# Performance work log

Hardware: AMD Instinct MI355X
Metric: run time of the kernel (lower is better)

Reference implementation:

```python
import jax, jax.numpy as jnp
import numpy as np

B, N, D_MODEL, HIDDEN = 4, 1024, 1024, 1024
N_HEAD, D_KEY, D_VALUE = 16, 64, 64


def setup_inputs() -> dict:
    key = jax.random.key(0)
    ks = jax.random.split(key, 12)
    s = 0.02
    return {
        "queries": jax.random.normal(ks[0], (B, N, D_MODEL), jnp.float32),
        "keys": jax.random.normal(ks[1], (B, N, HIDDEN), jnp.float32),
        "values": jax.random.normal(ks[2], (B, N, HIDDEN), jnp.float32),
        "attn_bias": jax.random.normal(ks[3], (B, N_HEAD, N, N), jnp.float32),
        "Wq": jax.random.normal(ks[4], (D_MODEL, D_KEY * N_HEAD), jnp.float32) * s,
        "bq": jnp.zeros((D_KEY * N_HEAD,), jnp.float32),
        "Wk": jax.random.normal(ks[5], (HIDDEN, D_KEY * N_HEAD), jnp.float32) * s,
        "bk": jnp.zeros((D_KEY * N_HEAD,), jnp.float32),
        "Wv": jax.random.normal(ks[6], (HIDDEN, D_VALUE * N_HEAD), jnp.float32) * s,
        "bv": jnp.zeros((D_VALUE * N_HEAD,), jnp.float32),
        "Wo": jax.random.normal(ks[7], (max(D_MODEL, HIDDEN), D_MODEL), jnp.float32) * s,
        "bo": jnp.zeros((D_MODEL,), jnp.float32),
    }


def reference(queries, keys, values, attn_bias, Wq, bq, Wk, bk, Wv, bv, Wo, bo):
    b, n, _ = queries.shape
    # QKV projections, split heads -> [b, h, n, d]
    q = (queries @ Wq + bq).reshape(b, n, N_HEAD, D_KEY).transpose(0, 2, 1, 3)
    k = (keys @ Wk + bk).reshape(b, keys.shape[1], N_HEAD, D_KEY).transpose(0, 2, 1, 3)
    v = (values @ Wv + bv).reshape(b, values.shape[1], N_HEAD, D_VALUE).transpose(0, 2, 1, 3)
    # scaled dot-product attention with additive bias (dropout_rate=0 -> identity)
    scaled_q = q * (D_KEY ** -0.5)
    product = jnp.einsum("bhqd,bhkd->bhqk", scaled_q, k) + attn_bias
    weights = jax.nn.softmax(product, axis=-1)
    ctx = jnp.einsum("bhqk,bhkd->bhqd", weights, v)
    # combine heads -> [b, n, h*d]
    out = ctx.transpose(0, 2, 1, 3).reshape(b, n, N_HEAD * D_VALUE)
    return out @ Wo + bo
```

## Files before the change

### kernel.cpp

```cpp
#include <hip/hip_runtime.h>
#include <cstdint>
#include <type_traits>


typedef unsigned short u16;
typedef __attribute__((ext_vector_type(8))) short v8bf;
typedef __attribute__((ext_vector_type(4))) float v4f;

#define DEV static __device__ __forceinline__

DEV u16 f2b(float f) {
    union { float f; uint32_t u; } v; v.f = f;
    uint32_t r = v.u + 0x7FFFu + ((v.u >> 16) & 1u);
    return (u16)(r >> 16);
}

DEV void gl_lds16(const void* g, void* l) {
    __builtin_amdgcn_global_load_lds((const __attribute__((address_space(1))) void*)g,
                                     (__attribute__((address_space(3))) void*)l, 16, 0, 0);
}

__global__ __launch_bounds__(256) void transpose_w4(const float* __restrict__ w0, const float* __restrict__ w1,
                                                    const float* __restrict__ w2, const float* __restrict__ w3,
                                                    u16* __restrict__ o0, u16* __restrict__ o1,
                                                    u16* __restrict__ o2, u16* __restrict__ o3) {
    __shared__ float tile[32][33];
    const float* in = blockIdx.z == 0 ? w0 : blockIdx.z == 1 ? w1 : blockIdx.z == 2 ? w2 : w3;
    u16* out        = blockIdx.z == 0 ? o0 : blockIdx.z == 1 ? o1 : blockIdx.z == 2 ? o2 : o3;
    const int tx = threadIdx.x, ty = threadIdx.y;
    const int n0 = blockIdx.x * 32, k0 = blockIdx.y * 32;
#pragma unroll
    for (int i = 0; i < 4; i++)
        tile[ty + i * 8][tx] = in[(size_t)(k0 + ty + i * 8) * 1024 + n0 + tx];
    __syncthreads();
#pragma unroll
    for (int i = 0; i < 4; i++)
        out[(size_t)(n0 + ty + i * 8) * 1024 + k0 + tx] = f2b(tile[tx][ty + i * 8]);
}

__global__ __launch_bounds__(256) void cast3(const float* __restrict__ a0, const float* __restrict__ a1,
                                             const float* __restrict__ a2,
                                             u16* __restrict__ o0, u16* __restrict__ o1, u16* __restrict__ o2) {
    const int z = blockIdx.y;
    const float* in = z == 0 ? a0 : z == 1 ? a1 : a2;
    u16* out        = z == 0 ? o0 : z == 1 ? o1 : o2;
    const size_t i = ((size_t)blockIdx.x * 256 + threadIdx.x) * 8;
    const float4 f0 = *reinterpret_cast<const float4*>(in + i);
    const float4 f1 = *reinterpret_cast<const float4*>(in + i + 4);
    union { u16 h[8]; uint4 v4; } pk;
    pk.h[0] = f2b(f0.x); pk.h[1] = f2b(f0.y); pk.h[2] = f2b(f0.z); pk.h[3] = f2b(f0.w);
    pk.h[4] = f2b(f1.x); pk.h[5] = f2b(f1.y); pk.h[6] = f2b(f1.z); pk.h[7] = f2b(f1.w);
    *reinterpret_cast<uint4*>(out + i) = pk.v4;
}

template <int BN, typename TO>
DEV void gemm_body(const u16* __restrict__ A, const u16* __restrict__ Bt,
                   const float* __restrict__ bias, TO* __restrict__ C,
                   u16* __restrict__ Ct, float cscale, bool storeT,
                   u16* aS, u16* bS) {
    constexpr int FJ = BN / 32;
    const int tid = threadIdx.x;
    const int wave = tid >> 6, lane = tid & 63, l16 = lane & 15, quad = lane >> 4;
    const int m0 = blockIdx.x * 128, n0 = blockIdx.y * BN;
    const int wr = wave >> 1, wc = wave & 1;
    const int r8 = lane >> 3, c8 = lane & 7;

    v4f acc[4][FJ];
#pragma unroll
    for (int i = 0; i < 4; i++)
#pragma unroll
        for (int j = 0; j < FJ; j++) acc[i][j] = (v4f){0.f, 0.f, 0.f, 0.f};

    for (int kk = 0; kk < 1024; kk += 64) {
        if (kk) __syncthreads();
#pragma unroll
        for (int cl = 0; cl < 4; cl++) {
            const int row = wave * 32 + cl * 8 + r8;
            gl_lds16(A + (size_t)(m0 + row) * 1024 + kk + ((c8 ^ (row & 7)) * 8),
                     aS + (wave * 32 + cl * 8) * 64);
        }
#pragma unroll
        for (int cl = 0; cl < BN / 32; cl++) {
            const int row = wave * (BN / 4) + cl * 8 + r8;
            gl_lds16(Bt + (size_t)(n0 + row) * 1024 + kk + ((c8 ^ (row & 7)) * 8),
                     bS + (wave * (BN / 4) + cl * 8) * 64);
        }
        __syncthreads();
#pragma unroll
        for (int kt = 0; kt < 2; kt++) {
            v8bf af[4], bf[FJ];
#pragma unroll
            for (int i = 0; i < 4; i++) {
                const int row = wr * 64 + i * 16 + l16;
                af[i] = *reinterpret_cast<const v8bf*>(aS + row * 64 + (((kt * 4 + quad) ^ (row & 7)) * 8));
            }
#pragma unroll
            for (int j = 0; j < FJ; j++) {
                const int row = wc * (BN / 2) + j * 16 + l16;
                bf[j] = *reinterpret_cast<const v8bf*>(bS + row * 64 + (((kt * 4 + quad) ^ (row & 7)) * 8));
            }
#pragma unroll
            for (int i = 0; i < 4; i++)
#pragma unroll
                for (int j = 0; j < FJ; j++)
                    acc[i][j] = __builtin_amdgcn_mfma_f32_16x16x32_bf16(af[i], bf[j], acc[i][j], 0, 0, 0);
        }
    }
    float bv[FJ];
#pragma unroll
    for (int j = 0; j < FJ; j++) bv[j] = bias[n0 + wc * (BN / 2) + j * 16 + l16];
    if (storeT) {
#pragma unroll
        for (int i = 0; i < 4; i++)
#pragma unroll
            for (int j = 0; j < FJ; j++) {
                const int col = n0 + wc * (BN / 2) + j * 16 + l16;
                const int row0 = m0 + wr * 64 + i * 16 + quad * 4;
                union { u16 h[4]; uint2 u; } pk;
#pragma unroll
                for (int r = 0; r < 4; r++) pk.h[r] = f2b((acc[i][j][r] + bv[j]) * cscale);
                *reinterpret_cast<uint2*>(&Ct[(size_t)col * 4096 + row0]) = pk.u;
            }
    } else {
#pragma unroll
        for (int i = 0; i < 4; i++)
#pragma unroll
            for (int j = 0; j < FJ; j++) {
                const int col = n0 + wc * (BN / 2) + j * 16 + l16;
#pragma unroll
                for (int r = 0; r < 4; r++) {
                    const int row = m0 + wr * 64 + i * 16 + quad * 4 + r;
                    const float val = (acc[i][j][r] + bv[j]) * cscale;
                    if constexpr (std::is_same_v<TO, u16>) C[(size_t)row * 1024 + col] = f2b(val);
                    else                                   C[(size_t)row * 1024 + col] = val;
                }
            }
    }
}

__global__ __launch_bounds__(256, 3) void gemm_qkv(
    const u16* __restrict__ Qc, const u16* __restrict__ Kc, const u16* __restrict__ Vc,
    const u16* __restrict__ WqT, const u16* __restrict__ WkT, const u16* __restrict__ WvT,
    const float* __restrict__ bq, const float* __restrict__ bk, const float* __restrict__ bv,
    u16* __restrict__ Qb, u16* __restrict__ Kb, u16* __restrict__ VT) {
    __shared__ __align__(16) u16 aS[128 * 64];
    __shared__ __align__(16) u16 bS[128 * 64];
    const int z = blockIdx.z;
    const u16* A    = z == 0 ? Qc : z == 1 ? Kc : Vc;
    const u16* Bt   = z == 0 ? WqT : z == 1 ? WkT : WvT;
    const float* bi = z == 0 ? bq : z == 1 ? bk : bv;
    u16* Cn         = z == 0 ? Qb : Kb;
    gemm_body<128, u16>(A, Bt, bi, Cn, VT, z == 0 ? 0.125f : 1.0f, z == 2, aS, bS);
}

__global__ __launch_bounds__(256, 3) void gemm_out(const u16* __restrict__ A, const u16* __restrict__ Bt,
                                                   const float* __restrict__ bias, float* __restrict__ C) {
    __shared__ __align__(16) u16 aS[128 * 64];
    __shared__ __align__(16) u16 bS[64 * 64];
    gemm_body<64, float>(A, Bt, bias, C, nullptr, 1.0f, false, aS, bS);
}

__global__ __launch_bounds__(256, 3) void attn2(const u16* __restrict__ Q,
                                                const u16* __restrict__ K,
                                                const u16* __restrict__ VT,
                                                const float* __restrict__ bias,
                                                u16* __restrict__ ctx) {
    __shared__ __align__(16) u16 kS[64 * 64];
    __shared__ __align__(16) u16 vS[64 * 64];
    __shared__ __align__(16) float biasS[64 * 64];
    __shared__ __align__(16) u16 pT[4][16 * 72];

    const int tid = threadIdx.x;
    const int wave = tid >> 6, lane = tid & 63, l16 = lane & 15, quad = lane >> 4;
    const int q0 = blockIdx.x * 64, bh = blockIdx.y, b = bh >> 4, h = bh & 15;
    const int r8 = lane >> 3, c8 = lane & 7;
    const int r16 = lane >> 4, c16 = lane & 15;

    v8bf qf[2];
    {
        const size_t qrow = ((size_t)(b * 1024 + q0 + wave * 16 + l16)) * 1024 + h * 64;
        qf[0] = *reinterpret_cast<const v8bf*>(Q + qrow + quad * 8);
        qf[1] = *reinterpret_cast<const v8bf*>(Q + qrow + 32 + quad * 8);
    }

    v4f ctxacc[4];
#pragma unroll
    for (int v = 0; v < 4; v++) ctxacc[v] = (v4f){0.f, 0.f, 0.f, 0.f};
    float rs = 0.f;

    const size_t kg = ((size_t)b * 1024) * 1024 + h * 64;
    const size_t vg = ((size_t)h * 64) * 4096 + b * 1024;
    const float* bp = bias + ((size_t)bh * 1024 + q0) * 1024;
    u16* pw = pT[wave];

    for (int c = 0; c < 16; c++) {
        const int nc = c * 64;
        if (c) __syncthreads();
#pragma unroll
        for (int cl = 0; cl < 2; cl++) {
            const int key = wave * 16 + cl * 8 + r8;
            gl_lds16(K + kg + (size_t)(nc + key) * 1024 + ((c8 ^ (key & 7)) * 8),
                     kS + (wave * 16 + cl * 8) * 64);
        }
#pragma unroll
        for (int cl = 0; cl < 2; cl++) {
            const int d = wave * 16 + cl * 8 + r8;
            gl_lds16(VT + vg + (size_t)d * 4096 + nc + ((c8 ^ (d & 7)) * 8),
                     vS + (wave * 16 + cl * 8) * 64);
        }
#pragma unroll
        for (int cl = 0; cl < 4; cl++) {
            const int row = wave * 16 + cl * 4 + r16;
            gl_lds16(bp + (size_t)row * 1024 + nc + ((c16 ^ (row & 15)) * 4),
                     biasS + (wave * 16 + cl * 4) * 64);
        }
        __syncthreads();

#pragma unroll
        for (int t = 0; t < 4; t++) {
            v4f s = (v4f){0.f, 0.f, 0.f, 0.f};
#pragma unroll
            for (int kt = 0; kt < 2; kt++) {
                const int krow = t * 16 + l16;
                const v8bf kf = *reinterpret_cast<const v8bf*>(
                    kS + krow * 64 + (((kt * 4 + quad) ^ (krow & 7)) * 8));
                s = __builtin_amdgcn_mfma_f32_16x16x32_bf16(kf, qf[kt], s, 0, 0, 0);
            }
            const float4 bi = *reinterpret_cast<const float4*>(
                biasS + (wave * 16 + l16) * 64 + (((t * 4 + quad) ^ l16) * 4));
            const float p0 = __expf(s[0] + bi.x);
            const float p1 = __expf(s[1] + bi.y);
            const float p2 = __expf(s[2] + bi.z);
            const float p3 = __expf(s[3] + bi.w);
            rs += (p0 + p1) + (p2 + p3);
            union { u16 h[4]; uint2 u; } pk;
            pk.h[0] = f2b(p0); pk.h[1] = f2b(p1); pk.h[2] = f2b(p2); pk.h[3] = f2b(p3);
            *reinterpret_cast<uint2*>(pw + l16 * 72 + t * 16 + quad * 4) = pk.u;
        }
#pragma unroll
        for (int kt = 0; kt < 2; kt++) {
            const v8bf pf = *reinterpret_cast<const v8bf*>(pw + l16 * 72 + kt * 32 + quad * 8);
#pragma unroll
            for (int v = 0; v < 4; v++) {
                const int drow = v * 16 + l16;
                const v8bf vf = *reinterpret_cast<const v8bf*>(
                    vS + drow * 64 + (((kt * 4 + quad) ^ (drow & 7)) * 8));
                ctxacc[v] = __builtin_amdgcn_mfma_f32_16x16x32_bf16(pf, vf, ctxacc[v], 0, 0, 0);
            }
        }
    }

    rs += __shfl_xor(rs, 16);
    rs += __shfl_xor(rs, 32);
    float dninv[4];
#pragma unroll
    for (int r = 0; r < 4; r++) dninv[r] = 1.f / __shfl(rs, quad * 4 + r, 16);
#pragma unroll
    for (int v = 0; v < 4; v++)
#pragma unroll
        for (int r = 0; r < 4; r++) {
            const int row = q0 + wave * 16 + quad * 4 + r;
            ctx[((size_t)(b * 1024 + row)) * 1024 + h * 64 + v * 16 + l16] =
                f2b(ctxacc[v][r] * dninv[r]);
        }
}

extern "C" void kernel_launch(void* const* d_in, const int* in_sizes, int n_in,
                              void* d_out, int out_size, void* d_ws, size_t ws_size,
                              hipStream_t stream) {
    const float* queries = (const float*)d_in[0];
    const float* keys    = (const float*)d_in[1];
    const float* values  = (const float*)d_in[2];
    const float* abias   = (const float*)d_in[3];
    const float* Wq = (const float*)d_in[4];
    const float* bq = (const float*)d_in[5];
    const float* Wk = (const float*)d_in[6];
    const float* bk = (const float*)d_in[7];
    const float* Wv = (const float*)d_in[8];
    const float* bv = (const float*)d_in[9];
    const float* Wo = (const float*)d_in[10];
    const float* bo = (const float*)d_in[11];
    float* out = (float*)d_out;

    char* ws = (char*)d_ws;
    u16* Qb   = (u16*)(ws);
    u16* Kb   = (u16*)(ws + (size_t)(8u << 20));
    u16* VTb  = (u16*)(ws + (size_t)(16u << 20));
    u16* ctxb = (u16*)(ws + (size_t)(24u << 20));
    u16* Qc   = (u16*)(ws + (size_t)(32u << 20));
    u16* Kc   = (u16*)(ws + (size_t)(40u << 20));
    u16* Vc   = (u16*)(ws + (size_t)(48u << 20));
    u16* WqT  = (u16*)(ws + (size_t)(56u << 20));
    u16* WkT  = (u16*)(ws + (size_t)(58u << 20));
    u16* WvT  = (u16*)(ws + (size_t)(60u << 20));
    u16* WoT  = (u16*)(ws + (size_t)(62u << 20));

    transpose_w4<<<dim3(32, 32, 4), dim3(32, 8), 0, stream>>>(Wq, Wk, Wv, Wo, WqT, WkT, WvT, WoT);
    cast3<<<dim3(2048, 3), 256, 0, stream>>>(queries, keys, values, Qc, Kc, Vc);
    gemm_qkv<<<dim3(32, 8, 3), 256, 0, stream>>>(Qc, Kc, Vc, WqT, WkT, WvT, bq, bk, bv, Qb, Kb, VTb);
    attn2<<<dim3(16, 64), 256, 0, stream>>>(Qb, Kb, VTb, abias, ctxb);
    gemm_out<<<dim3(32, 16), 256, 0, stream>>>(ctxb, WoT, bo, out);
}
```

Baseline: 491.0 us.

## Double-buffer K/V/bias LDS tiles in attention and add MFMA priority hints

The attention kernel now keeps two LDS buffers for the K, V^T and bias tiles. It issues the async global-to-LDS loads for the next key chunk before computing on the current one, so each chunk needs one barrier instead of two and load latency overlaps with MFMA and exp work. s_setprio is raised around the MFMA sequences, and the grid is reordered so the head/batch index varies fastest. The larger LDS footprint lowers the occupancy bound from 3 to 2 blocks per CU, which costs some latency hiding.

```diff
diff --git a/kernel.cpp b/kernel.cpp
--- a/kernel.cpp
+++ b/kernel.cpp
@@ -160,19 +160,20 @@
     gemm_body<64, float>(A, Bt, bias, C, nullptr, 1.0f, false, aS, bS);
 }
 
-__global__ __launch_bounds__(256, 3) void attn2(const u16* __restrict__ Q,
+__global__ __launch_bounds__(256, 2) void attn2(const u16* __restrict__ Q,
                                                 const u16* __restrict__ K,
                                                 const u16* __restrict__ VT,
                                                 const float* __restrict__ bias,
                                                 u16* __restrict__ ctx) {
-    __shared__ __align__(16) u16 kS[64 * 64];
-    __shared__ __align__(16) u16 vS[64 * 64];
-    __shared__ __align__(16) float biasS[64 * 64];
+    __shared__ __align__(16) u16 kS[2][64 * 64];
+    __shared__ __align__(16) u16 vS[2][64 * 64];
+    __shared__ __align__(16) float biasS[2][64 * 64];
     __shared__ __align__(16) u16 pT[4][16 * 72];
 
     const int tid = threadIdx.x;
     const int wave = tid >> 6, lane = tid & 63, l16 = lane & 15, quad = lane >> 4;
-    const int q0 = blockIdx.x * 64, bh = blockIdx.y, b = bh >> 4, h = bh & 15;
+    const int bh = blockIdx.x, q0 = blockIdx.y * 64;
+    const int b = bh >> 4, h = bh & 15;
     const int r8 = lane >> 3, c8 = lane & 7;
     const int r16 = lane >> 4, c16 = lane & 15;
 
@@ -193,41 +194,50 @@
     const float* bp = bias + ((size_t)bh * 1024 + q0) * 1024;
     u16* pw = pT[wave];
 
-    for (int c = 0; c < 16; c++) {
+    auto stage = [&](int c, int buf) {
         const int nc = c * 64;
-        if (c) __syncthreads();
 #pragma unroll
         for (int cl = 0; cl < 2; cl++) {
             const int key = wave * 16 + cl * 8 + r8;
             gl_lds16(K + kg + (size_t)(nc + key) * 1024 + ((c8 ^ (key & 7)) * 8),
-                     kS + (wave * 16 + cl * 8) * 64);
+                     kS[buf] + (wave * 16 + cl * 8) * 64);
         }
 #pragma unroll
         for (int cl = 0; cl < 2; cl++) {
             const int d = wave * 16 + cl * 8 + r8;
             gl_lds16(VT + vg + (size_t)d * 4096 + nc + ((c8 ^ (d & 7)) * 8),
-                     vS + (wave * 16 + cl * 8) * 64);
+                     vS[buf] + (wave * 16 + cl * 8) * 64);
         }
 #pragma unroll
         for (int cl = 0; cl < 4; cl++) {
             const int row = wave * 16 + cl * 4 + r16;
             gl_lds16(bp + (size_t)row * 1024 + nc + ((c16 ^ (row & 15)) * 4),
-                     biasS + (wave * 16 + cl * 4) * 64);
-        }
-        __syncthreads();
+                     biasS[buf] + (wave * 16 + cl * 4) * 64);
+        }
+    };
+
+    stage(0, 0);
+    asm volatile("s_waitcnt vmcnt(0)" ::: "memory");
+    __builtin_amdgcn_s_barrier();
+
+    for (int c = 0; c < 16; c++) {
+        const int buf = c & 1;
+        if (c < 15) stage(c + 1, buf ^ 1);
 
 #pragma unroll
         for (int t = 0; t < 4; t++) {
             v4f s = (v4f){0.f, 0.f, 0.f, 0.f};
+            __builtin_amdgcn_s_setprio(1);
 #pragma unroll
             for (int kt = 0; kt < 2; kt++) {
                 const int krow = t * 16 + l16;
                 const v8bf kf = *reinterpret_cast<const v8bf*>(
-                    kS + krow * 64 + (((kt * 4 + quad) ^ (krow & 7)) * 8));
+                    kS[buf] + krow * 64 + (((kt * 4 + quad) ^ (krow & 7)) * 8));
                 s = __builtin_amdgcn_mfma_f32_16x16x32_bf16(kf, qf[kt], s, 0, 0, 0);
             }
+            __builtin_amdgcn_s_setprio(0);
             const float4 bi = *reinterpret_cast<const float4*>(
-                biasS + (wave * 16 + l16) * 64 + (((t * 4 + quad) ^ l16) * 4));
+                biasS[buf] + (wave * 16 + l16) * 64 + (((t * 4 + quad) ^ l16) * 4));
             const float p0 = __expf(s[0] + bi.x);
             const float p1 = __expf(s[1] + bi.y);
             const float p2 = __expf(s[2] + bi.z);
@@ -240,13 +250,19 @@
 #pragma unroll
         for (int kt = 0; kt < 2; kt++) {
             const v8bf pf = *reinterpret_cast<const v8bf*>(pw + l16 * 72 + kt * 32 + quad * 8);
+            __builtin_amdgcn_s_setprio(1);
 #pragma unroll
             for (int v = 0; v < 4; v++) {
                 const int drow = v * 16 + l16;
                 const v8bf vf = *reinterpret_cast<const v8bf*>(
-                    vS + drow * 64 + (((kt * 4 + quad) ^ (drow & 7)) * 8));
+                    vS[buf] + drow * 64 + (((kt * 4 + quad) ^ (drow & 7)) * 8));
                 ctxacc[v] = __builtin_amdgcn_mfma_f32_16x16x32_bf16(pf, vf, ctxacc[v], 0, 0, 0);
             }
+            __builtin_amdgcn_s_setprio(0);
+        }
+        if (c < 15) {
+            asm volatile("s_waitcnt vmcnt(0)" ::: "memory");
+            __builtin_amdgcn_s_barrier();
         }
     }
 
@@ -298,6 +314,6 @@
     transpose_w4<<<dim3(32, 32, 4), dim3(32, 8), 0, stream>>>(Wq, Wk, Wv, Wo, WqT, WkT, WvT, WoT);
     cast3<<<dim3(2048, 3), 256, 0, stream>>>(queries, keys, values, Qc, Kc, Vc);
     gemm_qkv<<<dim3(32, 8, 3), 256, 0, stream>>>(Qc, Kc, Vc, WqT, WkT, WvT, bq, bk, bv, Qb, Kb, VTb);
-    attn2<<<dim3(16, 64), 256, 0, stream>>>(Qb, Kb, VTb, abias, ctxb);
+    attn2<<<dim3(64, 16), 256, 0, stream>>>(Qb, Kb, VTb, abias, ctxb);
     gemm_out<<<dim3(32, 16), 256, 0, stream>>>(ctxb, WoT, bo, out);
 }
```

After: 493.6 us. No clear change (+0.5%).
